# Performance work log

Measured on AMD Instinct MI355X. Metric: run time of the kernel, lower is better.

Reference implementation:

```python
import jax, jax.numpy as jnp
import numpy as np

B, R, T, Q = 4096, 130, 200, 64  # batch, ROIs, BOLD length (= feature_nums), query dim
EPS = 1e-5
GCN_DIMS = [(T, 16), (16, 16), (16, 4), (4, 4), (4, 2), (2, 2)]


def bn1d(x, g, b):
    # torch.nn.BatchNorm1d(R) on (B, R, L): channel dim=1, training-mode batch stats, biased var
    m = x.mean(axis=(0, 2), keepdims=True)
    v = ((x - m) ** 2).mean(axis=(0, 2), keepdims=True)
    return g[None, :, None] * (x - m) * jax.lax.rsqrt(v + EPS) + b[None, :, None]


def setup_inputs() -> dict:
    key = jax.random.key(0)
    ks = jax.random.split(key, 16)

    def kaiming(k, shape, fan_in):  # kaiming_normal_ with relu gain
        return (jax.random.normal(k, shape) * np.sqrt(2.0 / fan_in)).astype(jnp.float32)

    inp = {}
    inp['BOLD_signals'] = jax.random.normal(ks[0], (B, R, T), dtype=jnp.float32)
    inp['threshold'] = jnp.float32(0.005)
    inp['wq'] = kaiming(ks[1], (Q, T), T)
    inp['bq'] = jnp.zeros((Q,), jnp.float32)
    inp['g_t'] = jnp.ones((R,), jnp.float32)
    inp['b_t'] = jnp.zeros((R,), jnp.float32)
    for i, (fi, fo) in enumerate(GCN_DIMS, 1):
        inp[f'w{i}'] = kaiming(ks[1 + i], (fo, fi), fi)
        inp[f'b{i}'] = jnp.zeros((fo,), jnp.float32)
        inp[f'g{i}'] = jnp.ones((R,), jnp.float32)
        inp[f'beta{i}'] = jnp.zeros((R,), jnp.float32)
    inp['w_mlp'] = kaiming(ks[9], (2, R * 2), R * 2)
    inp['b_mlp'] = jnp.zeros((2,), jnp.float32)
    return inp


def reference(BOLD_signals, threshold, wq, bq, g_t, b_t,
              w1, b1, g1, beta1, w2, b2, g2, beta2, w3, b3, g3, beta3,
              w4, b4, g4, beta4, w5, b5, g5, beta5, w6, b6, g6, beta6,
              w_mlp, b_mlp):
    x = jnp.where(jnp.isnan(BOLD_signals), 0.0, BOLD_signals)  # (B,R,T)

    # Transformer-style relation matrix (note: K is a reshape, not a transpose, per source)
    qk = x @ wq.T + bq                      # (B,R,Q)
    Qm = qk.reshape(-1, R, Q)               # (B,R,Q)
    Km = qk.reshape(-1, Q, R)               # (B,Q,R)  -- faithful reshape
    rel = jnp.einsum('brq,bqs->brs', Qm, Km)  # (B,R,R)
    rel = bn1d(rel, g_t, b_t)
    rel = jax.nn.softmax(rel, axis=2)
    rel = jax.nn.relu(rel - threshold)

    def gcn(A, f, w, b, g, beta):
        return jax.nn.relu(bn1d(A @ f @ w.T + b, g, beta))

    h = gcn(rel, x, w1, b1, g1, beta1)           # (B,R,16)
    h = gcn(rel, h, w2, b2, g2, beta2) + h       # res
    h = gcn(rel, h, w3, b3, g3, beta3)           # (B,R,4)
    h = gcn(rel, h, w4, b4, g4, beta4) + h       # res
    h = gcn(rel, h, w5, b5, g5, beta5)           # (B,R,2)
    h = gcn(rel, h, w6, b6, g6, beta6) + h       # res

    out = jax.nn.relu(h.reshape(h.shape[0], -1) @ w_mlp.T + b_mlp)  # (B,2)
    return out
```

## Files before the change

### kernel.cpp

```cpp
#include <hip/hip_runtime.h>
#include <math.h>


typedef _Float16 f16;
typedef _Float16 f16x8 __attribute__((ext_vector_type(8)));
typedef _Float16 f16x4 __attribute__((ext_vector_type(4)));
typedef float f32x4 __attribute__((ext_vector_type(4)));

#define MFMA16(a, b, c) __builtin_amdgcn_mfma_f32_16x16x32_f16((a), (b), (c), 0, 0, 0)

__global__ __launch_bounds__(256) void w_prep(
    const float* __restrict__ wq, const float* __restrict__ w1, f16* __restrict__ wf)
{
  const int f = blockIdx.x;
  const int k = threadIdx.x;
  if (k < 224) {
    float v = 0.f;
    if (k < 200) v = (f < 64) ? wq[f * 200 + k] : w1[(f - 64) * 200 + k];
    wf[f * 224 + k] = (f16)v;
  }
}

__global__ __launch_bounds__(256) void k_in(
    const float* __restrict__ x, const f16* __restrict__ wf,
    const float* __restrict__ bq, f16* __restrict__ qk, f16* __restrict__ xw1)
{
  __shared__ f16 xs[64 * 232];
  const int tid = threadIdx.x;
  const size_t m0 = (size_t)blockIdx.x * 64;
  {
    int r = tid >> 2, j = tid & 3;
    *(float4*)&xs[r * 232 + 200 + j * 8] = make_float4(0, 0, 0, 0);
  }
  const float4* xsrc = (const float4*)(x + m0 * 200);
  for (int i = tid; i < 3200; i += 256) {
    int r = i / 50, c = i - (i / 50) * 50;
    float4 v = xsrc[i];
    v.x = (v.x != v.x) ? 0.f : v.x;
    v.y = (v.y != v.y) ? 0.f : v.y;
    v.z = (v.z != v.z) ? 0.f : v.z;
    v.w = (v.w != v.w) ? 0.f : v.w;
    f16x4 h; h[0] = (f16)v.x; h[1] = (f16)v.y; h[2] = (f16)v.z; h[3] = (f16)v.w;
    *(f16x4*)&xs[r * 232 + c * 4] = h;
  }
  __syncthreads();
  const int lane = tid & 63, wv = tid >> 6;
  const int mrow = lane & 15, quad = lane >> 4;
  f32x4 acc[5];
#pragma unroll
  for (int n = 0; n < 5; n++) acc[n] = (f32x4){0.f, 0.f, 0.f, 0.f};
  const f16* xrow = &xs[(wv * 16 + mrow) * 232 + quad * 8];
  const f16* wrow = wf + mrow * 224 + quad * 8;
#pragma unroll
  for (int k0 = 0; k0 < 224; k0 += 32) {
    f16x8 af = *(const f16x8*)(xrow + k0);
#pragma unroll
    for (int n = 0; n < 5; n++)
      acc[n] = MFMA16(af, *(const f16x8*)(wrow + n * 3584 + k0), acc[n]);
  }
  const size_t rbase = m0 + wv * 16;
#pragma unroll
  for (int n = 0; n < 4; n++) {
    int col = n * 16 + mrow;
    float bqv = bq[col];
#pragma unroll
    for (int i = 0; i < 4; i++)
      qk[(rbase + quad * 4 + i) * 64 + col] = (f16)(acc[n][i] + bqv);
  }
#pragma unroll
  for (int i = 0; i < 4; i++)
    xw1[(rbase + quad * 4 + i) * 16 + mrow] = (f16)acc[4][i];
}

__device__ __forceinline__ void gather_bfrags(const f16* qf, int mrow, int quad,
                                              f16x8 bf[9][2])
{
#pragma unroll
  for (int n = 0; n < 9; n++) {
    const int s = n * 16 + mrow;
    const bool ok = (s < 130);
#pragma unroll
    for (int kh = 0; kh < 2; kh++) {
      f16x8 t;
#pragma unroll
      for (int j = 0; j < 8; j++) {
        int q = kh * 32 + quad * 8 + j;
        t[j] = ok ? qf[q * 130 + s] : (f16)0.f;
      }
      bf[n][kh] = t;
    }
  }
}

__global__ __launch_bounds__(256) void k_relstats(
    const f16* __restrict__ qk, float* __restrict__ sp)
{
  __shared__ f16 qf[8320];
  const int b = blockIdx.x, tid = threadIdx.x;
  const f16* qb = qk + (size_t)b * 8320;
  for (int i = tid; i < 1040; i += 256)
    *(f16x8*)&qf[i * 8] = *(const f16x8*)(qb + i * 8);
  __syncthreads();
  const int lane = tid & 63, wv = tid >> 6, mrow = lane & 15, quad = lane >> 4;
  f16x8 bf[9][2];
  gather_bfrags(qf, mrow, quad, bf);
  for (int m = wv; m < 9; m += 4) {
    const f16* arow = qb + (m * 16 + mrow) * 64 + quad * 8;
    f16x8 af0 = *(const f16x8*)arow;
    f16x8 af1 = *(const f16x8*)(arow + 32);
    float p1[4] = {0, 0, 0, 0}, p2[4] = {0, 0, 0, 0};
#pragma unroll
    for (int n = 0; n < 9; n++) {
      f32x4 acc = (f32x4){0.f, 0.f, 0.f, 0.f};
      acc = MFMA16(af0, bf[n][0], acc);
      acc = MFMA16(af1, bf[n][1], acc);
#pragma unroll
      for (int i = 0; i < 4; i++) { float v = acc[i]; p1[i] += v; p2[i] += v * v; }
    }
#pragma unroll
    for (int i = 0; i < 4; i++)
#pragma unroll
      for (int msk = 1; msk <= 8; msk <<= 1) {
        p1[i] += __shfl_xor(p1[i], msk); p2[i] += __shfl_xor(p2[i], msk);
      }
    if (mrow == 0) {
#pragma unroll
      for (int i = 0; i < 4; i++) {
        int r = m * 16 + quad * 4 + i;
        if (r < 130) {
          sp[(size_t)r * 4096 + b] = p1[i];
          sp[130 * 4096 + (size_t)r * 4096 + b] = p2[i];
        }
      }
    }
  }
}

__global__ __launch_bounds__(256) void k_stats(
    const float* __restrict__ sp, const float* __restrict__ g,
    const float* __restrict__ beta, float invN, float* __restrict__ ac)
{
  const int r = blockIdx.x, tid = threadIdx.x;
  float s1 = 0.f, s2 = 0.f;
  const float* p1 = sp + (size_t)r * 4096;
  const float* p2 = sp + 130 * 4096 + (size_t)r * 4096;
  for (int j = tid; j < 4096; j += 256) { s1 += p1[j]; s2 += p2[j]; }
#pragma unroll
  for (int m = 1; m <= 32; m <<= 1) { s1 += __shfl_xor(s1, m); s2 += __shfl_xor(s2, m); }
  __shared__ float r1[4], r2[4];
  if ((tid & 63) == 0) { r1[tid >> 6] = s1; r2[tid >> 6] = s2; }
  __syncthreads();
  if (tid == 0) {
    float S1 = r1[0] + r1[1] + r1[2] + r1[3];
    float S2 = r2[0] + r2[1] + r2[2] + r2[3];
    float mean = S1 * invN;
    float var = S2 * invN - mean * mean;
    float a = g[r] * rsqrtf(var + 1e-5f);
    ac[r] = a;
    ac[130 + r] = beta[r] - mean * a;
  }
}

__global__ __launch_bounds__(256) void k_Asoft(
    const f16* __restrict__ qk, const float* __restrict__ ac0,
    const float* __restrict__ thrp, f16* __restrict__ A16)
{
  __shared__ f16 qf[8320];
  const int b = blockIdx.x, tid = threadIdx.x;
  const f16* qb = qk + (size_t)b * 8320;
  for (int i = tid; i < 1040; i += 256)
    *(f16x8*)&qf[i * 8] = *(const f16x8*)(qb + i * 8);
  __syncthreads();
  const float thr = *thrp;
  const int lane = tid & 63, wv = tid >> 6, mrow = lane & 15, quad = lane >> 4;
  f16x8 bf[9][2];
  gather_bfrags(qf, mrow, quad, bf);
  f16* Ab = A16 + (size_t)b * 17680;
  for (int m = wv; m < 9; m += 4) {
    float a4[4], c4[4];
#pragma unroll
    for (int i = 0; i < 4; i++) {
      int r = m * 16 + quad * 4 + i;
      a4[i] = (r < 130) ? ac0[r] : 0.f;
      c4[i] = (r < 130) ? ac0[130 + r] : 0.f;
    }
    const f16* arow = qb + (m * 16 + mrow) * 64 + quad * 8;
    f16x8 af0 = *(const f16x8*)arow;
    f16x8 af1 = *(const f16x8*)(arow + 32);
    f32x4 acc[9];
#pragma unroll
    for (int n = 0; n < 9; n++) {
      acc[n] = (f32x4){0.f, 0.f, 0.f, 0.f};
      acc[n] = MFMA16(af0, bf[n][0], acc[n]);
      acc[n] = MFMA16(af1, bf[n][1], acc[n]);
    }
    float mx[4] = {-3e38f, -3e38f, -3e38f, -3e38f}, sm[4] = {0, 0, 0, 0};
#pragma unroll
    for (int n = 0; n < 9; n++) {
      const bool valid = (n * 16 + mrow) < 130;
#pragma unroll
      for (int i = 0; i < 4; i++) {
        float v = a4[i] * acc[n][i] + c4[i];
        float ve = valid ? v : -3e38f;
        float nm = fmaxf(mx[i], ve);
        sm[i] = sm[i] * __expf(mx[i] - nm) + (valid ? __expf(v - nm) : 0.f);
        mx[i] = nm;
      }
    }
#pragma unroll
    for (int i = 0; i < 4; i++) {
#pragma unroll
      for (int msk = 1; msk <= 8; msk <<= 1) {
        float om = __shfl_xor(mx[i], msk), os = __shfl_xor(sm[i], msk);
        float nm = fmaxf(mx[i], om);
        sm[i] = sm[i] * __expf(mx[i] - nm) + os * __expf(om - nm);
        mx[i] = nm;
      }
      sm[i] = 1.f / sm[i];
    }
#pragma unroll
    for (int n = 0; n < 9; n++) {
      const int col = n * 16 + mrow;
#pragma unroll
      for (int i = 0; i < 4; i++) {
        int r = m * 16 + quad * 4 + i;
        if (r < 130) {
          if (col < 130) {
            float v = a4[i] * acc[n][i] + c4[i];
            Ab[r * 136 + col] = (f16)fmaxf(__expf(v - mx[i]) * sm[i] - thr, 0.f);
          } else if (col < 136) {
            Ab[r * 136 + col] = (f16)0.f;
          }
        }
      }
    }
  }
}

template <int FI, int FO, bool RES, bool G1>
__global__ __launch_bounds__(256) void k_gcn(
    const f16* __restrict__ A16, const float* __restrict__ ZP,
    const float* __restrict__ ZQ, const f16* __restrict__ xw1,
    const float* __restrict__ acP, const float* __restrict__ acQ,
    const float* __restrict__ wmat, const float* __restrict__ bb,
    float* __restrict__ Zout, float* __restrict__ sp)
{
  __shared__ f16 gT[16 * 168];
  const int b = blockIdx.x, tid = threadIdx.x;
  for (int i = tid; i < 1344; i += 256) ((float*)gT)[i] = 0.f;
  __syncthreads();
  if constexpr (G1) {
    for (int i = tid; i < 2080; i += 256) {
      int s = i >> 4, f = i & 15;
      gT[f * 168 + s] = xw1[(size_t)b * 2080 + i];
    }
  } else {
    if (tid < 130) {
      const int r = tid;
      float h[FI];
      const float* zp = ZP + ((size_t)b * 130 + r) * FI;
      const float aP = acP[r], cP = acP[130 + r];
#pragma unroll
      for (int i = 0; i < FI; i++) h[i] = fmaxf(aP * zp[i] + cP, 0.f);
      if constexpr (RES) {
        const float* zq = ZQ + ((size_t)b * 130 + r) * FI;
        const float aQ = acQ[r], cQ = acQ[130 + r];
#pragma unroll
        for (int i = 0; i < FI; i++) h[i] += fmaxf(aQ * zq[i] + cQ, 0.f);
      }
#pragma unroll
      for (int k = 0; k < FO; k++) {
        float s = 0.f;
#pragma unroll
        for (int i = 0; i < FI; i++) s += h[i] * wmat[k * FI + i];
        gT[k * 168 + r] = (f16)s;
      }
    }
  }
  __syncthreads();
  const int lane = tid & 63, wv = tid >> 6, mrow = lane & 15, quad = lane >> 4;
  f16x8 bfr[5];
#pragma unroll
  for (int kk = 0; kk < 5; kk++)
    bfr[kk] = *(const f16x8*)&gT[mrow * 168 + kk * 32 + quad * 8];
  const f16* Ab = A16 + (size_t)b * 17680;
  for (int m = wv; m < 9; m += 4) {
    const f16* arow = Ab + (m * 16 + mrow) * 136 + quad * 8;
    f32x4 acc = (f32x4){0.f, 0.f, 0.f, 0.f};
#pragma unroll
    for (int kk = 0; kk < 5; kk++)
      acc = MFMA16(*(const f16x8*)(arow + kk * 32), bfr[kk], acc);
    const int col = mrow;
    const float bk = (col < FO) ? bb[col] : 0.f;
    float p1[4], p2[4];
#pragma unroll
    for (int i = 0; i < 4; i++) {
      int r = m * 16 + quad * 4 + i;
      float v = (col < FO) ? acc[i] + bk : 0.f;
      if (col < FO && r < 130)
        Zout[((size_t)b * 130 + r) * FO + col] = v;
      p1[i] = v; p2[i] = v * v;
    }
#pragma unroll
    for (int i = 0; i < 4; i++)
#pragma unroll
      for (int msk = 1; msk <= 8; msk <<= 1) {
        p1[i] += __shfl_xor(p1[i], msk); p2[i] += __shfl_xor(p2[i], msk);
      }
    if (mrow == 0) {
#pragma unroll
      for (int i = 0; i < 4; i++) {
        int r = m * 16 + quad * 4 + i;
        if (r < 130) {
          sp[(size_t)r * 4096 + b] = p1[i];
          sp[130 * 4096 + (size_t)r * 4096 + b] = p2[i];
        }
      }
    }
  }
}

__global__ __launch_bounds__(256) void k_mlp(
    const float* __restrict__ Z5, const float* __restrict__ Z6,
    const float* __restrict__ ac5, const float* __restrict__ ac6,
    const float* __restrict__ wm, const float* __restrict__ bm, float* __restrict__ out)
{
  const int tid = threadIdx.x, lane = tid & 63, wv = tid >> 6;
  const int b = blockIdx.x * 4 + wv;
  const float* z5 = Z5 + (size_t)b * 260;
  const float* z6 = Z6 + (size_t)b * 260;
  float p0 = 0.f, p1 = 0.f;
#pragma unroll
  for (int j = 0; j < 5; j++) {
    int i = lane + 64 * j;
    if (i < 260) {
      int r = i >> 1;
      float h = fmaxf(ac6[r] * z6[i] + ac6[130 + r], 0.f)
              + fmaxf(ac5[r] * z5[i] + ac5[130 + r], 0.f);
      p0 += h * wm[i];
      p1 += h * wm[260 + i];
    }
  }
#pragma unroll
  for (int m = 1; m <= 32; m <<= 1) { p0 += __shfl_xor(p0, m); p1 += __shfl_xor(p1, m); }
  if (lane == 0) {
    out[(size_t)b * 2] = fmaxf(p0 + bm[0], 0.f);
    out[(size_t)b * 2 + 1] = fmaxf(p1 + bm[1], 0.f);
  }
}

extern "C" void kernel_launch(void* const* d_in, const int* in_sizes, int n_in,
                              void* d_out, int out_size, void* d_ws, size_t ws_size,
                              hipStream_t stream) {
  const float* X   = (const float*)d_in[0];
  const float* THR = (const float*)d_in[1];
  const float* WQ  = (const float*)d_in[2];
  const float* BQ  = (const float*)d_in[3];
  const float* GT  = (const float*)d_in[4];
  const float* BT  = (const float*)d_in[5];
  const float* W1 = (const float*)d_in[6];  const float* Bb1 = (const float*)d_in[7];
  const float* G1g = (const float*)d_in[8]; const float* BE1 = (const float*)d_in[9];
  const float* W2 = (const float*)d_in[10]; const float* Bb2 = (const float*)d_in[11];
  const float* G2 = (const float*)d_in[12]; const float* BE2 = (const float*)d_in[13];
  const float* W3 = (const float*)d_in[14]; const float* Bb3 = (const float*)d_in[15];
  const float* G3 = (const float*)d_in[16]; const float* BE3 = (const float*)d_in[17];
  const float* W4 = (const float*)d_in[18]; const float* Bb4 = (const float*)d_in[19];
  const float* G4 = (const float*)d_in[20]; const float* BE4 = (const float*)d_in[21];
  const float* W5 = (const float*)d_in[22]; const float* Bb5 = (const float*)d_in[23];
  const float* G5 = (const float*)d_in[24]; const float* BE5 = (const float*)d_in[25];
  const float* W6 = (const float*)d_in[26]; const float* Bb6 = (const float*)d_in[27];
  const float* G6 = (const float*)d_in[28]; const float* BE6 = (const float*)d_in[29];
  const float* WM = (const float*)d_in[30]; const float* BM = (const float*)d_in[31];

  float* ws = (float*)d_ws;
  f16*   A16   = (f16*)ws;
  f16*   qk16  = (f16*)(ws + 36208640);
  f16*   xw116 = (f16*)(ws + 53248000);
  f16*   wf16  = (f16*)(ws + 57507840);
  float* Z1 = ws + 57516800;
  float* Z2 = ws + 66036480;
  float* Z3 = ws + 74556160;
  float* Z4 = ws + 76686080;
  float* Z5 = ws + 78816000;
  float* Z6 = ws + 79880960;
  float* sp = ws + 80945920;
  float* ac = ws + 82010880;

  w_prep<<<80, 256, 0, stream>>>(WQ, W1, wf16);
  k_in<<<8320, 256, 0, stream>>>(X, wf16, BQ, qk16, xw116);
  k_relstats<<<4096, 256, 0, stream>>>(qk16, sp);
  k_stats<<<130, 256, 0, stream>>>(sp, GT, BT, 1.f / 532480.f, ac);
  k_Asoft<<<4096, 256, 0, stream>>>(qk16, ac, THR, A16);
  k_gcn<16, 16, false, true><<<4096, 256, 0, stream>>>(A16, nullptr, nullptr, xw116,
      nullptr, nullptr, nullptr, Bb1, Z1, sp);
  k_stats<<<130, 256, 0, stream>>>(sp, G1g, BE1, 1.f / 65536.f, ac + 260);
  k_gcn<16, 16, false, false><<<4096, 256, 0, stream>>>(A16, Z1, nullptr, nullptr,
      ac + 260, nullptr, W2, Bb2, Z2, sp);
  k_stats<<<130, 256, 0, stream>>>(sp, G2, BE2, 1.f / 65536.f, ac + 520);
  k_gcn<16, 4, true, false><<<4096, 256, 0, stream>>>(A16, Z2, Z1, nullptr,
      ac + 520, ac + 260, W3, Bb3, Z3, sp);
  k_stats<<<130, 256, 0, stream>>>(sp, G3, BE3, 1.f / 16384.f, ac + 780);
  k_gcn<4, 4, false, false><<<4096, 256, 0, stream>>>(A16, Z3, nullptr, nullptr,
      ac + 780, nullptr, W4, Bb4, Z4, sp);
  k_stats<<<130, 256, 0, stream>>>(sp, G4, BE4, 1.f / 16384.f, ac + 1040);
  k_gcn<4, 2, true, false><<<4096, 256, 0, stream>>>(A16, Z4, Z3, nullptr,
      ac + 1040, ac + 780, W5, Bb5, Z5, sp);
  k_stats<<<130, 256, 0, stream>>>(sp, G5, BE5, 1.f / 8192.f, ac + 1300);
  k_gcn<2, 2, false, false><<<4096, 256, 0, stream>>>(A16, Z5, nullptr, nullptr,
      ac + 1300, nullptr, W6, Bb6, Z6, sp);
  k_stats<<<130, 256, 0, stream>>>(sp, G6, BE6, 1.f / 8192.f, ac + 1560);
  k_mlp<<<1024, 256, 0, stream>>>(Z5, Z6, ac + 1300, ac + 1560, WM, BM, (float*)d_out);
}
```

Before: 1.136 ms.

## Fuse all stages into one persistent cooperative kernel with grid syncs

Replaces the sequence of separate kernel launches with a single cooperative persistent kernel. Blocks loop over work items and use grid-wide barriers between phases, which removes per-launch overhead and tail gaps between the many small stats and GCN kernels. The input projection now reads X directly from global memory instead of staging it in LDS. The softmax is reworked into a three-pass recompute (max, sum, write) that repeats the small MFMAs instead of keeping all accumulators in registers. In exchange, occupancy is capped at a fixed grid, the 130-block stats phases leave most blocks idle at barriers, and the extra MFMA passes add compute.

```diff
diff --git a/kernel.cpp b/kernel.cpp
--- a/kernel.cpp
+++ b/kernel.cpp
@@ -1,76 +1,29 @@
 #include <hip/hip_runtime.h>
+#include <hip/hip_cooperative_groups.h>
 #include <math.h>
+
+namespace cg = cooperative_groups;
 
 
 typedef _Float16 f16;
 typedef _Float16 f16x8 __attribute__((ext_vector_type(8)));
-typedef _Float16 f16x4 __attribute__((ext_vector_type(4)));
 typedef float f32x4 __attribute__((ext_vector_type(4)));
 
 #define MFMA16(a, b, c) __builtin_amdgcn_mfma_f32_16x16x32_f16((a), (b), (c), 0, 0, 0)
 
-__global__ __launch_bounds__(256) void w_prep(
-    const float* __restrict__ wq, const float* __restrict__ w1, f16* __restrict__ wf)
-{
-  const int f = blockIdx.x;
-  const int k = threadIdx.x;
-  if (k < 224) {
-    float v = 0.f;
-    if (k < 200) v = (f < 64) ? wq[f * 200 + k] : w1[(f - 64) * 200 + k];
-    wf[f * 224 + k] = (f16)v;
-  }
-}
-
-__global__ __launch_bounds__(256) void k_in(
-    const float* __restrict__ x, const f16* __restrict__ wf,
-    const float* __restrict__ bq, f16* __restrict__ qk, f16* __restrict__ xw1)
-{
-  __shared__ f16 xs[64 * 232];
-  const int tid = threadIdx.x;
-  const size_t m0 = (size_t)blockIdx.x * 64;
-  {
-    int r = tid >> 2, j = tid & 3;
-    *(float4*)&xs[r * 232 + 200 + j * 8] = make_float4(0, 0, 0, 0);
-  }
-  const float4* xsrc = (const float4*)(x + m0 * 200);
-  for (int i = tid; i < 3200; i += 256) {
-    int r = i / 50, c = i - (i / 50) * 50;
-    float4 v = xsrc[i];
-    v.x = (v.x != v.x) ? 0.f : v.x;
-    v.y = (v.y != v.y) ? 0.f : v.y;
-    v.z = (v.z != v.z) ? 0.f : v.z;
-    v.w = (v.w != v.w) ? 0.f : v.w;
-    f16x4 h; h[0] = (f16)v.x; h[1] = (f16)v.y; h[2] = (f16)v.z; h[3] = (f16)v.w;
-    *(f16x4*)&xs[r * 232 + c * 4] = h;
-  }
-  __syncthreads();
-  const int lane = tid & 63, wv = tid >> 6;
-  const int mrow = lane & 15, quad = lane >> 4;
-  f32x4 acc[5];
-#pragma unroll
-  for (int n = 0; n < 5; n++) acc[n] = (f32x4){0.f, 0.f, 0.f, 0.f};
-  const f16* xrow = &xs[(wv * 16 + mrow) * 232 + quad * 8];
-  const f16* wrow = wf + mrow * 224 + quad * 8;
-#pragma unroll
-  for (int k0 = 0; k0 < 224; k0 += 32) {
-    f16x8 af = *(const f16x8*)(xrow + k0);
-#pragma unroll
-    for (int n = 0; n < 5; n++)
-      acc[n] = MFMA16(af, *(const f16x8*)(wrow + n * 3584 + k0), acc[n]);
-  }
-  const size_t rbase = m0 + wv * 16;
-#pragma unroll
-  for (int n = 0; n < 4; n++) {
-    int col = n * 16 + mrow;
-    float bqv = bq[col];
-#pragma unroll
-    for (int i = 0; i < 4; i++)
-      qk[(rbase + quad * 4 + i) * 64 + col] = (f16)(acc[n][i] + bqv);
-  }
-#pragma unroll
-  for (int i = 0; i < 4; i++)
-    xw1[(rbase + quad * 4 + i) * 16 + mrow] = (f16)acc[4][i];
-}
+struct Params {
+  const float *X, *THR, *WQ, *BQ, *GT, *BT;
+  const float *W1, *Bb1, *G1, *BE1;
+  const float *W2, *Bb2, *G2, *BE2;
+  const float *W3, *Bb3, *G3, *BE3;
+  const float *W4, *Bb4, *G4, *BE4;
+  const float *W5, *Bb5, *G5, *BE5;
+  const float *W6, *Bb6, *G6, *BE6;
+  const float *WM, *BM;
+  f16 *A16, *qk, *xw1, *wf;
+  float *Z1, *Z2, *Z3, *Z4, *Z5, *Z6, *sp, *ac;
+  float *out;
+};
 
 __device__ __forceinline__ void gather_bfrags(const f16* qf, int mrow, int quad,
                                               f16x8 bf[9][2])
@@ -92,144 +45,289 @@
   }
 }
 
-__global__ __launch_bounds__(256) void k_relstats(
-    const f16* __restrict__ qk, float* __restrict__ sp)
-{
-  __shared__ f16 qf[8320];
-  const int b = blockIdx.x, tid = threadIdx.x;
-  const f16* qb = qk + (size_t)b * 8320;
-  for (int i = tid; i < 1040; i += 256)
-    *(f16x8*)&qf[i * 8] = *(const f16x8*)(qb + i * 8);
-  __syncthreads();
+__device__ void kin_phase(const float* __restrict__ X, const f16* __restrict__ wf,
+                          const float* __restrict__ bq, f16* __restrict__ qk,
+                          f16* __restrict__ xw1, int bid, int nb, int tid)
+{
   const int lane = tid & 63, wv = tid >> 6, mrow = lane & 15, quad = lane >> 4;
-  f16x8 bf[9][2];
-  gather_bfrags(qf, mrow, quad, bf);
-  for (int m = wv; m < 9; m += 4) {
-    const f16* arow = qb + (m * 16 + mrow) * 64 + quad * 8;
-    f16x8 af0 = *(const f16x8*)arow;
-    f16x8 af1 = *(const f16x8*)(arow + 32);
-    float p1[4] = {0, 0, 0, 0}, p2[4] = {0, 0, 0, 0};
-#pragma unroll
-    for (int n = 0; n < 9; n++) {
-      f32x4 acc = (f32x4){0.f, 0.f, 0.f, 0.f};
-      acc = MFMA16(af0, bf[n][0], acc);
-      acc = MFMA16(af1, bf[n][1], acc);
-#pragma unroll
-      for (int i = 0; i < 4; i++) { float v = acc[i]; p1[i] += v; p2[i] += v * v; }
+  const int cbase = quad * 8;
+  for (int t = bid; t < 8320; t += nb) {
+    const size_t m0 = (size_t)t * 64;
+    const float* xr = X + (m0 + wv * 16 + mrow) * 200;
+    f32x4 acc[5];
+#pragma unroll
+    for (int n = 0; n < 5; n++) acc[n] = (f32x4){0.f, 0.f, 0.f, 0.f};
+#pragma unroll
+    for (int k0 = 0; k0 < 224; k0 += 32) {
+      const int c0 = k0 + cbase;
+      f16x8 af;
+#pragma unroll
+      for (int j = 0; j < 8; j++) af[j] = (f16)0.f;
+      if (c0 < 200) {
+        float4 v0 = *(const float4*)(xr + c0);
+        float4 v1 = *(const float4*)(xr + c0 + 4);
+        float vv[8];
+        *(float4*)&vv[0] = v0;
+        *(float4*)&vv[4] = v1;
+#pragma unroll
+        for (int j = 0; j < 8; j++) {
+          float x = vv[j];
+          af[j] = (f16)((x != x) ? 0.f : x);
+        }
+      }
+#pragma unroll
+      for (int n = 0; n < 5; n++)
+        acc[n] = MFMA16(af, *(const f16x8*)(wf + (n * 16 + mrow) * 224 + c0), acc[n]);
+    }
+    const size_t rbase = m0 + wv * 16;
+#pragma unroll
+    for (int n = 0; n < 4; n++) {
+      int col = n * 16 + mrow;
+      float bqv = bq[col];
+#pragma unroll
+      for (int i = 0; i < 4; i++)
+        qk[(rbase + quad * 4 + i) * 64 + col] = (f16)(acc[n][i] + bqv);
     }
 #pragma unroll
     for (int i = 0; i < 4; i++)
-#pragma unroll
-      for (int msk = 1; msk <= 8; msk <<= 1) {
-        p1[i] += __shfl_xor(p1[i], msk); p2[i] += __shfl_xor(p2[i], msk);
-      }
-    if (mrow == 0) {
+      xw1[(rbase + quad * 4 + i) * 16 + mrow] = (f16)acc[4][i];
+  }
+}
+
+__device__ void relstats_phase(const f16* __restrict__ qk, float* __restrict__ sp,
+                               f16* qf, int bid, int nb, int tid)
+{
+  const int lane = tid & 63, wv = tid >> 6, mrow = lane & 15, quad = lane >> 4;
+  for (int b = bid; b < 4096; b += nb) {
+    __syncthreads();
+    const f16* qb = qk + (size_t)b * 8320;
+    for (int i = tid; i < 1040; i += 256)
+      *(f16x8*)&qf[i * 8] = *(const f16x8*)(qb + i * 8);
+    __syncthreads();
+    f16x8 bf[9][2];
+    gather_bfrags(qf, mrow, quad, bf);
+    for (int m = wv; m < 9; m += 4) {
+      const f16* arow = qb + (m * 16 + mrow) * 64 + quad * 8;
+      f16x8 af0 = *(const f16x8*)arow;
+      f16x8 af1 = *(const f16x8*)(arow + 32);
+      float p1[4] = {0, 0, 0, 0}, p2[4] = {0, 0, 0, 0};
+#pragma unroll
+      for (int n = 0; n < 9; n++) {
+        f32x4 acc = (f32x4){0.f, 0.f, 0.f, 0.f};
+        acc = MFMA16(af0, bf[n][0], acc);
+        acc = MFMA16(af1, bf[n][1], acc);
+#pragma unroll
+        for (int i = 0; i < 4; i++) { float v = acc[i]; p1[i] += v; p2[i] += v * v; }
+      }
+#pragma unroll
+      for (int i = 0; i < 4; i++)
+#pragma unroll
+        for (int msk = 1; msk <= 8; msk <<= 1) {
+          p1[i] += __shfl_xor(p1[i], msk); p2[i] += __shfl_xor(p2[i], msk);
+        }
+      if (mrow == 0) {
+#pragma unroll
+        for (int i = 0; i < 4; i++) {
+          int r = m * 16 + quad * 4 + i;
+          if (r < 130) {
+            sp[(size_t)r * 4096 + b] = p1[i];
+            sp[130 * 4096 + (size_t)r * 4096 + b] = p2[i];
+          }
+        }
+      }
+    }
+  }
+}
+
+__device__ void stats_phase(const float* __restrict__ sp, const float* __restrict__ g,
+                            const float* __restrict__ be, float invN,
+                            float* __restrict__ acOut, float* rr, int bid, int tid)
+{
+  if (bid < 130) {
+    const int r = bid;
+    float s1 = 0.f, s2 = 0.f;
+    const float* p1 = sp + (size_t)r * 4096;
+    const float* p2 = sp + 130 * 4096 + (size_t)r * 4096;
+    for (int j = tid; j < 4096; j += 256) { s1 += p1[j]; s2 += p2[j]; }
+#pragma unroll
+    for (int m = 1; m <= 32; m <<= 1) { s1 += __shfl_xor(s1, m); s2 += __shfl_xor(s2, m); }
+    if ((tid & 63) == 0) { rr[tid >> 6] = s1; rr[4 + (tid >> 6)] = s2; }
+    __syncthreads();
+    if (tid == 0) {
+      float S1 = rr[0] + rr[1] + rr[2] + rr[3];
+      float S2 = rr[4] + rr[5] + rr[6] + rr[7];
+      float mean = S1 * invN;
+      float var = S2 * invN - mean * mean;
+      float a = g[r] * rsqrtf(var + 1e-5f);
+      acOut[r] = a;
+      acOut[130 + r] = be[r] - mean * a;
+    }
+  }
+}
+
+__device__ void asoft_phase(const f16* __restrict__ qk, const float* __restrict__ ac0,
+                            float thr, f16* __restrict__ A16, f16* qf,
+                            int bid, int nb, int tid)
+{
+  const int lane = tid & 63, wv = tid >> 6, mrow = lane & 15, quad = lane >> 4;
+  for (int b = bid; b < 4096; b += nb) {
+    __syncthreads();
+    const f16* qb = qk + (size_t)b * 8320;
+    for (int i = tid; i < 1040; i += 256)
+      *(f16x8*)&qf[i * 8] = *(const f16x8*)(qb + i * 8);
+    __syncthreads();
+    f16x8 bf[9][2];
+    gather_bfrags(qf, mrow, quad, bf);
+    f16* Ab = A16 + (size_t)b * 17680;
+    for (int m = wv; m < 9; m += 4) {
+      float a4[4], c4[4];
 #pragma unroll
       for (int i = 0; i < 4; i++) {
         int r = m * 16 + quad * 4 + i;
-        if (r < 130) {
-          sp[(size_t)r * 4096 + b] = p1[i];
-          sp[130 * 4096 + (size_t)r * 4096 + b] = p2[i];
-        }
-      }
-    }
-  }
-}
-
-__global__ __launch_bounds__(256) void k_stats(
-    const float* __restrict__ sp, const float* __restrict__ g,
-    const float* __restrict__ beta, float invN, float* __restrict__ ac)
-{
-  const int r = blockIdx.x, tid = threadIdx.x;
-  float s1 = 0.f, s2 = 0.f;
-  const float* p1 = sp + (size_t)r * 4096;
-  const float* p2 = sp + 130 * 4096 + (size_t)r * 4096;
-  for (int j = tid; j < 4096; j += 256) { s1 += p1[j]; s2 += p2[j]; }
-#pragma unroll
-  for (int m = 1; m <= 32; m <<= 1) { s1 += __shfl_xor(s1, m); s2 += __shfl_xor(s2, m); }
-  __shared__ float r1[4], r2[4];
-  if ((tid & 63) == 0) { r1[tid >> 6] = s1; r2[tid >> 6] = s2; }
-  __syncthreads();
-  if (tid == 0) {
-    float S1 = r1[0] + r1[1] + r1[2] + r1[3];
-    float S2 = r2[0] + r2[1] + r2[2] + r2[3];
-    float mean = S1 * invN;
-    float var = S2 * invN - mean * mean;
-    float a = g[r] * rsqrtf(var + 1e-5f);
-    ac[r] = a;
-    ac[130 + r] = beta[r] - mean * a;
-  }
-}
-
-__global__ __launch_bounds__(256) void k_Asoft(
-    const f16* __restrict__ qk, const float* __restrict__ ac0,
-    const float* __restrict__ thrp, f16* __restrict__ A16)
-{
-  __shared__ f16 qf[8320];
-  const int b = blockIdx.x, tid = threadIdx.x;
-  const f16* qb = qk + (size_t)b * 8320;
-  for (int i = tid; i < 1040; i += 256)
-    *(f16x8*)&qf[i * 8] = *(const f16x8*)(qb + i * 8);
-  __syncthreads();
-  const float thr = *thrp;
+        a4[i] = (r < 130) ? ac0[r] : 0.f;
+        c4[i] = (r < 130) ? ac0[130 + r] : 0.f;
+      }
+      const f16* arow = qb + (m * 16 + mrow) * 64 + quad * 8;
+      f16x8 af0 = *(const f16x8*)arow;
+      f16x8 af1 = *(const f16x8*)(arow + 32);
+      float mx[4] = {-3e38f, -3e38f, -3e38f, -3e38f};
+#pragma unroll
+      for (int n = 0; n < 9; n++) {
+        f32x4 acc = (f32x4){0.f, 0.f, 0.f, 0.f};
+        acc = MFMA16(af0, bf[n][0], acc);
+        acc = MFMA16(af1, bf[n][1], acc);
+        const bool valid = (n * 16 + mrow) < 130;
+#pragma unroll
+        for (int i = 0; i < 4; i++) {
+          float v = a4[i] * acc[i] + c4[i];
+          if (valid) mx[i] = fmaxf(mx[i], v);
+        }
+      }
+#pragma unroll
+      for (int i = 0; i < 4; i++)
+#pragma unroll
+        for (int msk = 1; msk <= 8; msk <<= 1)
+          mx[i] = fmaxf(mx[i], __shfl_xor(mx[i], msk));
+      float sm[4] = {0.f, 0.f, 0.f, 0.f};
+#pragma unroll
+      for (int n = 0; n < 9; n++) {
+        f32x4 acc = (f32x4){0.f, 0.f, 0.f, 0.f};
+        acc = MFMA16(af0, bf[n][0], acc);
+        acc = MFMA16(af1, bf[n][1], acc);
+        const bool valid = (n * 16 + mrow) < 130;
+#pragma unroll
+        for (int i = 0; i < 4; i++) {
+          float v = a4[i] * acc[i] + c4[i];
+          if (valid) sm[i] += __expf(v - mx[i]);
+        }
+      }
+#pragma unroll
+      for (int i = 0; i < 4; i++) {
+#pragma unroll
+        for (int msk = 1; msk <= 8; msk <<= 1)
+          sm[i] += __shfl_xor(sm[i], msk);
+        sm[i] = 1.f / sm[i];
+      }
+#pragma unroll
+      for (int n = 0; n < 9; n++) {
+        f32x4 acc = (f32x4){0.f, 0.f, 0.f, 0.f};
+        acc = MFMA16(af0, bf[n][0], acc);
+        acc = MFMA16(af1, bf[n][1], acc);
+        const int col = n * 16 + mrow;
+#pragma unroll
+        for (int i = 0; i < 4; i++) {
+          int r = m * 16 + quad * 4 + i;
+          if (r < 130) {
+            if (col < 130) {
+              float v = a4[i] * acc[i] + c4[i];
+              Ab[r * 136 + col] = (f16)fmaxf(__expf(v - mx[i]) * sm[i] - thr, 0.f);
+            } else if (col < 136) {
+              Ab[r * 136 + col] = (f16)0.f;
+            }
+          }
+        }
+      }
+    }
+  }
+}
+
+template <int FI, int FO, bool RES, bool G1f>
+__device__ void gcn_phase(const f16* __restrict__ A16, const float* __restrict__ ZP,
+                          const float* __restrict__ ZQ, const f16* __restrict__ xw1,
+                          const float* __restrict__ acP, const float* __restrict__ acQ,
+                          const float* __restrict__ wmat, const float* __restrict__ bb,
+                          float* __restrict__ Zout, float* __restrict__ sp,
+                          f16* gT, int bid, int nb, int tid)
+{
   const int lane = tid & 63, wv = tid >> 6, mrow = lane & 15, quad = lane >> 4;
-  f16x8 bf[9][2];
-  gather_bfrags(qf, mrow, quad, bf);
-  f16* Ab = A16 + (size_t)b * 17680;
-  for (int m = wv; m < 9; m += 4) {
-    float a4[4], c4[4];
-#pragma unroll
-    for (int i = 0; i < 4; i++) {
-      int r = m * 16 + quad * 4 + i;
-      a4[i] = (r < 130) ? ac0[r] : 0.f;
-      c4[i] = (r < 130) ? ac0[130 + r] : 0.f;
-    }
-    const f16* arow = qb + (m * 16 + mrow) * 64 + quad * 8;
-    f16x8 af0 = *(const f16x8*)arow;
-    f16x8 af1 = *(const f16x8*)(arow + 32);
-    f32x4 acc[9];
-#pragma unroll
-    for (int n = 0; n < 9; n++) {
-      acc[n] = (f32x4){0.f, 0.f, 0.f, 0.f};
-      acc[n] = MFMA16(af0, bf[n][0], acc[n]);
-      acc[n] = MFMA16(af1, bf[n][1], acc[n]);
-    }
-    float mx[4] = {-3e38f, -3e38f, -3e38f, -3e38f}, sm[4] = {0, 0, 0, 0};
-#pragma unroll
-    for (int n = 0; n < 9; n++) {
-      const bool valid = (n * 16 + mrow) < 130;
-#pragma unroll
-      for (int i = 0; i < 4; i++) {
-        float v = a4[i] * acc[n][i] + c4[i];
-        float ve = valid ? v : -3e38f;
-        float nm = fmaxf(mx[i], ve);
-        sm[i] = sm[i] * __expf(mx[i] - nm) + (valid ? __expf(v - nm) : 0.f);
-        mx[i] = nm;
-      }
-    }
-#pragma unroll
-    for (int i = 0; i < 4; i++) {
-#pragma unroll
-      for (int msk = 1; msk <= 8; msk <<= 1) {
-        float om = __shfl_xor(mx[i], msk), os = __shfl_xor(sm[i], msk);
-        float nm = fmaxf(mx[i], om);
-        sm[i] = sm[i] * __expf(mx[i] - nm) + os * __expf(om - nm);
-        mx[i] = nm;
-      }
-      sm[i] = 1.f / sm[i];
-    }
-#pragma unroll
-    for (int n = 0; n < 9; n++) {
-      const int col = n * 16 + mrow;
+  for (int b = bid; b < 4096; b += nb) {
+    __syncthreads();
+    for (int i = tid; i < 1344; i += 256) ((float*)gT)[i] = 0.f;
+    __syncthreads();
+    if constexpr (G1f) {
+      for (int i = tid; i < 2080; i += 256) {
+        int s = i >> 4, f = i & 15;
+        gT[f * 168 + s] = xw1[(size_t)b * 2080 + i];
+      }
+    } else {
+      if (tid < 130) {
+        const int r = tid;
+        float h[FI];
+        const float* zp = ZP + ((size_t)b * 130 + r) * FI;
+        const float aP = acP[r], cP = acP[130 + r];
+#pragma unroll
+        for (int i = 0; i < FI; i++) h[i] = fmaxf(aP * zp[i] + cP, 0.f);
+        if constexpr (RES) {
+          const float* zq = ZQ + ((size_t)b * 130 + r) * FI;
+          const float aQ = acQ[r], cQ = acQ[130 + r];
+#pragma unroll
+          for (int i = 0; i < FI; i++) h[i] += fmaxf(aQ * zq[i] + cQ, 0.f);
+        }
+#pragma unroll
+        for (int k = 0; k < FO; k++) {
+          float s = 0.f;
+#pragma unroll
+          for (int i = 0; i < FI; i++) s += h[i] * wmat[k * FI + i];
+          gT[k * 168 + r] = (f16)s;
+        }
+      }
+    }
+    __syncthreads();
+    f16x8 bfr[5];
+#pragma unroll
+    for (int kk = 0; kk < 5; kk++)
+      bfr[kk] = *(const f16x8*)&gT[mrow * 168 + kk * 32 + quad * 8];
+    const f16* Ab = A16 + (size_t)b * 17680;
+    for (int m = wv; m < 9; m += 4) {
+      const f16* arow = Ab + (m * 16 + mrow) * 136 + quad * 8;
+      f32x4 acc = (f32x4){0.f, 0.f, 0.f, 0.f};
+#pragma unroll
+      for (int kk = 0; kk < 5; kk++)
+        acc = MFMA16(*(const f16x8*)(arow + kk * 32), bfr[kk], acc);
+      const int col = mrow;
+      const float bk = (col < FO) ? bb[col] : 0.f;
+      float p1[4], p2[4];
 #pragma unroll
       for (int i = 0; i < 4; i++) {
         int r = m * 16 + quad * 4 + i;
-        if (r < 130) {
-          if (col < 130) {
-            float v = a4[i] * acc[n][i] + c4[i];
-            Ab[r * 136 + col] = (f16)fmaxf(__expf(v - mx[i]) * sm[i] - thr, 0.f);
-          } else if (col < 136) {
-            Ab[r * 136 + col] = (f16)0.f;
+        float v = (col < FO) ? acc[i] + bk : 0.f;
+        if (col < FO && r < 130)
+          Zout[((size_t)b * 130 + r) * FO + col] = v;
+        p1[i] = v; p2[i] = v * v;
+      }
+#pragma unroll
+      for (int i = 0; i < 4; i++)
+#pragma unroll
+        for (int msk = 1; msk <= 8; msk <<= 1) {
+          p1[i] += __shfl_xor(p1[i], msk); p2[i] += __shfl_xor(p2[i], msk);
+        }
+      if (mrow == 0) {
+#pragma unroll
+        for (int i = 0; i < 4; i++) {
+          int r = m * 16 + quad * 4 + i;
+          if (r < 130) {
+            sp[(size_t)r * 4096 + b] = p1[i];
+            sp[130 * 4096 + (size_t)r * 4096 + b] = p2[i];
           }
         }
       }
@@ -237,177 +335,138 @@
   }
 }
 
-template <int FI, int FO, bool RES, bool G1>
-__global__ __launch_bounds__(256) void k_gcn(
-    const f16* __restrict__ A16, const float* __restrict__ ZP,
-    const float* __restrict__ ZQ, const f16* __restrict__ xw1,
-    const float* __restrict__ acP, const float* __restrict__ acQ,
-    const float* __restrict__ wmat, const float* __restrict__ bb,
-    float* __restrict__ Zout, float* __restrict__ sp)
-{
-  __shared__ f16 gT[16 * 168];
-  const int b = blockIdx.x, tid = threadIdx.x;
-  for (int i = tid; i < 1344; i += 256) ((float*)gT)[i] = 0.f;
-  __syncthreads();
-  if constexpr (G1) {
-    for (int i = tid; i < 2080; i += 256) {
-      int s = i >> 4, f = i & 15;
-      gT[f * 168 + s] = xw1[(size_t)b * 2080 + i];
-    }
-  } else {
-    if (tid < 130) {
-      const int r = tid;
-      float h[FI];
-      const float* zp = ZP + ((size_t)b * 130 + r) * FI;
-      const float aP = acP[r], cP = acP[130 + r];
-#pragma unroll
-      for (int i = 0; i < FI; i++) h[i] = fmaxf(aP * zp[i] + cP, 0.f);
-      if constexpr (RES) {
-        const float* zq = ZQ + ((size_t)b * 130 + r) * FI;
-        const float aQ = acQ[r], cQ = acQ[130 + r];
-#pragma unroll
-        for (int i = 0; i < FI; i++) h[i] += fmaxf(aQ * zq[i] + cQ, 0.f);
-      }
-#pragma unroll
-      for (int k = 0; k < FO; k++) {
-        float s = 0.f;
-#pragma unroll
-        for (int i = 0; i < FI; i++) s += h[i] * wmat[k * FI + i];
-        gT[k * 168 + r] = (f16)s;
-      }
-    }
-  }
-  __syncthreads();
-  const int lane = tid & 63, wv = tid >> 6, mrow = lane & 15, quad = lane >> 4;
-  f16x8 bfr[5];
-#pragma unroll
-  for (int kk = 0; kk < 5; kk++)
-    bfr[kk] = *(const f16x8*)&gT[mrow * 168 + kk * 32 + quad * 8];
-  const f16* Ab = A16 + (size_t)b * 17680;
-  for (int m = wv; m < 9; m += 4) {
-    const f16* arow = Ab + (m * 16 + mrow) * 136 + quad * 8;
-    f32x4 acc = (f32x4){0.f, 0.f, 0.f, 0.f};
-#pragma unroll
-    for (int kk = 0; kk < 5; kk++)
-      acc = MFMA16(*(const f16x8*)(arow + kk * 32), bfr[kk], acc);
-    const int col = mrow;
-    const float bk = (col < FO) ? bb[col] : 0.f;
-    float p1[4], p2[4];
-#pragma unroll
-    for (int i = 0; i < 4; i++) {
-      int r = m * 16 + quad * 4 + i;
-      float v = (col < FO) ? acc[i] + bk : 0.f;
-      if (col < FO && r < 130)
-        Zout[((size_t)b * 130 + r) * FO + col] = v;
-      p1[i] = v; p2[i] = v * v;
-    }
-#pragma unroll
-    for (int i = 0; i < 4; i++)
-#pragma unroll
-      for (int msk = 1; msk <= 8; msk <<= 1) {
-        p1[i] += __shfl_xor(p1[i], msk); p2[i] += __shfl_xor(p2[i], msk);
-      }
-    if (mrow == 0) {
-#pragma unroll
-      for (int i = 0; i < 4; i++) {
-        int r = m * 16 + quad * 4 + i;
-        if (r < 130) {
-          sp[(size_t)r * 4096 + b] = p1[i];
-          sp[130 * 4096 + (size_t)r * 4096 + b] = p2[i];
-        }
-      }
-    }
-  }
-}
-
-__global__ __launch_bounds__(256) void k_mlp(
-    const float* __restrict__ Z5, const float* __restrict__ Z6,
-    const float* __restrict__ ac5, const float* __restrict__ ac6,
-    const float* __restrict__ wm, const float* __restrict__ bm, float* __restrict__ out)
-{
-  const int tid = threadIdx.x, lane = tid & 63, wv = tid >> 6;
-  const int b = blockIdx.x * 4 + wv;
-  const float* z5 = Z5 + (size_t)b * 260;
-  const float* z6 = Z6 + (size_t)b * 260;
-  float p0 = 0.f, p1 = 0.f;
-#pragma unroll
-  for (int j = 0; j < 5; j++) {
-    int i = lane + 64 * j;
-    if (i < 260) {
-      int r = i >> 1;
-      float h = fmaxf(ac6[r] * z6[i] + ac6[130 + r], 0.f)
-              + fmaxf(ac5[r] * z5[i] + ac5[130 + r], 0.f);
-      p0 += h * wm[i];
-      p1 += h * wm[260 + i];
-    }
-  }
-#pragma unroll
-  for (int m = 1; m <= 32; m <<= 1) { p0 += __shfl_xor(p0, m); p1 += __shfl_xor(p1, m); }
-  if (lane == 0) {
-    out[(size_t)b * 2] = fmaxf(p0 + bm[0], 0.f);
-    out[(size_t)b * 2 + 1] = fmaxf(p1 + bm[1], 0.f);
-  }
+__device__ void mlp_phase(const float* __restrict__ Z5, const float* __restrict__ Z6,
+                          const float* __restrict__ ac5, const float* __restrict__ ac6,
+                          const float* __restrict__ wm, const float* __restrict__ bm,
+                          float* __restrict__ out, int bid, int nb, int tid)
+{
+  const int lane = tid & 63, wv = tid >> 6;
+  for (int b = bid * 4 + wv; b < 4096; b += nb * 4) {
+    const float* z5 = Z5 + (size_t)b * 260;
+    const float* z6 = Z6 + (size_t)b * 260;
+    float p0 = 0.f, p1 = 0.f;
+#pragma unroll
+    for (int j = 0; j < 5; j++) {
+      int i = lane + 64 * j;
+      if (i < 260) {
+        int r = i >> 1;
+        float h = fmaxf(ac6[r] * z6[i] + ac6[130 + r], 0.f)
+                + fmaxf(ac5[r] * z5[i] + ac5[130 + r], 0.f);
+        p0 += h * wm[i];
+        p1 += h * wm[260 + i];
+      }
+    }
+#pragma unroll
+    for (int m = 1; m <= 32; m <<= 1) { p0 += __shfl_xor(p0, m); p1 += __shfl_xor(p1, m); }
+    if (lane == 0) {
+      out[(size_t)b * 2] = fmaxf(p0 + bm[0], 0.f);
+      out[(size_t)b * 2 + 1] = fmaxf(p1 + bm[1], 0.f);
+    }
+  }
+}
+
+__global__ __launch_bounds__(256, 4) void mega(Params P, int nb)
+{
+  cg::grid_group grid = cg::this_grid();
+  __shared__ __align__(16) char smemraw[16640];
+  f16* qf = (f16*)smemraw;
+  f16* gT = (f16*)smemraw;
+  float* rr = (float*)smemraw;
+  const int bid = blockIdx.x, tid = threadIdx.x;
+
+  for (int idx = bid * 256 + tid; idx < 80 * 224; idx += nb * 256) {
+    int f = idx / 224, k = idx - f * 224;
+    float v = 0.f;
+    if (k < 200) v = (f < 64) ? P.WQ[f * 200 + k] : P.W1[(f - 64) * 200 + k];
+    P.wf[idx] = (f16)v;
+  }
+  grid.sync();
+  kin_phase(P.X, P.wf, P.BQ, P.qk, P.xw1, bid, nb, tid);
+  grid.sync();
+  relstats_phase(P.qk, P.sp, qf, bid, nb, tid);
+  grid.sync();
+  stats_phase(P.sp, P.GT, P.BT, 1.f / 532480.f, P.ac, rr, bid, tid);
+  grid.sync();
+  const float thr = *P.THR;
+  asoft_phase(P.qk, P.ac, thr, P.A16, qf, bid, nb, tid);
+  grid.sync();
+  gcn_phase<16, 16, false, true>(P.A16, nullptr, nullptr, P.xw1, nullptr, nullptr,
+                                 nullptr, P.Bb1, P.Z1, P.sp, gT, bid, nb, tid);
+  grid.sync();
+  stats_phase(P.sp, P.G1, P.BE1, 1.f / 65536.f, P.ac + 260, rr, bid, tid);
+  grid.sync();
+  gcn_phase<16, 16, false, false>(P.A16, P.Z1, nullptr, nullptr, P.ac + 260, nullptr,
+                                  P.W2, P.Bb2, P.Z2, P.sp, gT, bid, nb, tid);
+  grid.sync();
+  stats_phase(P.sp, P.G2, P.BE2, 1.f / 65536.f, P.ac + 520, rr, bid, tid);
+  grid.sync();
+  gcn_phase<16, 4, true, false>(P.A16, P.Z2, P.Z1, nullptr, P.ac + 520, P.ac + 260,
+                                P.W3, P.Bb3, P.Z3, P.sp, gT, bid, nb, tid);
+  grid.sync();
+  stats_phase(P.sp, P.G3, P.BE3, 1.f / 16384.f, P.ac + 780, rr, bid, tid);
+  grid.sync();
+  gcn_phase<4, 4, false, false>(P.A16, P.Z3, nullptr, nullptr, P.ac + 780, nullptr,
+                                P.W4, P.Bb4, P.Z4, P.sp, gT, bid, nb, tid);
+  grid.sync();
+  stats_phase(P.sp, P.G4, P.BE4, 1.f / 16384.f, P.ac + 1040, rr, bid, tid);
+  grid.sync();
+  gcn_phase<4, 2, true, false>(P.A16, P.Z4, P.Z3, nullptr, P.ac + 1040, P.ac + 780,
+                               P.W5, P.Bb5, P.Z5, P.sp, gT, bid, nb, tid);
+  grid.sync();
+  stats_phase(P.sp, P.G5, P.BE5, 1.f / 8192.f, P.ac + 1300, rr, bid, tid);
+  grid.sync();
+  gcn_phase<2, 2, false, false>(P.A16, P.Z5, nullptr, nullptr, P.ac + 1300, nullptr,
+                                P.W6, P.Bb6, P.Z6, P.sp, gT, bid, nb, tid);
+  grid.sync();
+  stats_phase(P.sp, P.G6, P.BE6, 1.f / 8192.f, P.ac + 1560, rr, bid, tid);
+  grid.sync();
+  mlp_phase(P.Z5, P.Z6, P.ac + 1300, P.ac + 1560, P.WM, P.BM, P.out, bid, nb, tid);
 }
 
 extern "C" void kernel_launch(void* const* d_in, const int* in_sizes, int n_in,
                               void* d_out, int out_size, void* d_ws, size_t ws_size,
                               hipStream_t stream) {
-  const float* X   = (const float*)d_in[0];
-  const float* THR = (const float*)d_in[1];
-  const float* WQ  = (const float*)d_in[2];
-  const float* BQ  = (const float*)d_in[3];
-  const float* GT  = (const float*)d_in[4];
-  const float* BT  = (const float*)d_in[5];
-  const float* W1 = (const float*)d_in[6];  const float* Bb1 = (const float*)d_in[7];
-  const float* G1g = (const float*)d_in[8]; const float* BE1 = (const float*)d_in[9];
-  const float* W2 = (const float*)d_in[10]; const float* Bb2 = (const float*)d_in[11];
-  const float* G2 = (const float*)d_in[12]; const float* BE2 = (const float*)d_in[13];
-  const float* W3 = (const float*)d_in[14]; const float* Bb3 = (const float*)d_in[15];
-  const float* G3 = (const float*)d_in[16]; const float* BE3 = (const float*)d_in[17];
-  const float* W4 = (const float*)d_in[18]; const float* Bb4 = (const float*)d_in[19];
-  const float* G4 = (const float*)d_in[20]; const float* BE4 = (const float*)d_in[21];
-  const float* W5 = (const float*)d_in[22]; const float* Bb5 = (const float*)d_in[23];
-  const float* G5 = (const float*)d_in[24]; const float* BE5 = (const float*)d_in[25];
-  const float* W6 = (const float*)d_in[26]; const float* Bb6 = (const float*)d_in[27];
-  const float* G6 = (const float*)d_in[28]; const float* BE6 = (const float*)d_in[29];
-  const float* WM = (const float*)d_in[30]; const float* BM = (const float*)d_in[31];
+  Params P;
+  P.X   = (const float*)d_in[0];
+  P.THR = (const float*)d_in[1];
+  P.WQ  = (const float*)d_in[2];
+  P.BQ  = (const float*)d_in[3];
+  P.GT  = (const float*)d_in[4];
+  P.BT  = (const float*)d_in[5];
+  P.W1 = (const float*)d_in[6];  P.Bb1 = (const float*)d_in[7];
+  P.G1 = (const float*)d_in[8];  P.BE1 = (const float*)d_in[9];
+  P.W2 = (const float*)d_in[10]; P.Bb2 = (const float*)d_in[11];
+  P.G2 = (const float*)d_in[12]; P.BE2 = (const float*)d_in[13];
+  P.W3 = (const float*)d_in[14]; P.Bb3 = (const float*)d_in[15];
+  P.G3 = (const float*)d_in[16]; P.BE3 = (const float*)d_in[17];
+  P.W4 = (const float*)d_in[18]; P.Bb4 = (const float*)d_in[19];
+  P.G4 = (const float*)d_in[20]; P.BE4 = (const float*)d_in[21];
+  P.W5 = (const float*)d_in[22]; P.Bb5 = (const float*)d_in[23];
+  P.G5 = (const float*)d_in[24]; P.BE5 = (const float*)d_in[25];
+  P.W6 = (const float*)d_in[26]; P.Bb6 = (const float*)d_in[27];
+  P.G6 = (const float*)d_in[28]; P.BE6 = (const float*)d_in[29];
+  P.WM = (const float*)d_in[30]; P.BM = (const float*)d_in[31];
 
   float* ws = (float*)d_ws;
-  f16*   A16   = (f16*)ws;
-  f16*   qk16  = (f16*)(ws + 36208640);
-  f16*   xw116 = (f16*)(ws + 53248000);
-  f16*   wf16  = (f16*)(ws + 57507840);
-  float* Z1 = ws + 57516800;
-  float* Z2 = ws + 66036480;
-  float* Z3 = ws + 74556160;
-  float* Z4 = ws + 76686080;
-  float* Z5 = ws + 78816000;
-  float* Z6 = ws + 79880960;
-  float* sp = ws + 80945920;
-  float* ac = ws + 82010880;
-
-  w_prep<<<80, 256, 0, stream>>>(WQ, W1, wf16);
-  k_in<<<8320, 256, 0, stream>>>(X, wf16, BQ, qk16, xw116);
-  k_relstats<<<4096, 256, 0, stream>>>(qk16, sp);
-  k_stats<<<130, 256, 0, stream>>>(sp, GT, BT, 1.f / 532480.f, ac);
-  k_Asoft<<<4096, 256, 0, stream>>>(qk16, ac, THR, A16);
-  k_gcn<16, 16, false, true><<<4096, 256, 0, stream>>>(A16, nullptr, nullptr, xw116,
-      nullptr, nullptr, nullptr, Bb1, Z1, sp);
-  k_stats<<<130, 256, 0, stream>>>(sp, G1g, BE1, 1.f / 65536.f, ac + 260);
-  k_gcn<16, 16, false, false><<<4096, 256, 0, stream>>>(A16, Z1, nullptr, nullptr,
-      ac + 260, nullptr, W2, Bb2, Z2, sp);
-  k_stats<<<130, 256, 0, stream>>>(sp, G2, BE2, 1.f / 65536.f, ac + 520);
-  k_gcn<16, 4, true, false><<<4096, 256, 0, stream>>>(A16, Z2, Z1, nullptr,
-      ac + 520, ac + 260, W3, Bb3, Z3, sp);
-  k_stats<<<130, 256, 0, stream>>>(sp, G3, BE3, 1.f / 16384.f, ac + 780);
-  k_gcn<4, 4, false, false><<<4096, 256, 0, stream>>>(A16, Z3, nullptr, nullptr,
-      ac + 780, nullptr, W4, Bb4, Z4, sp);
-  k_stats<<<130, 256, 0, stream>>>(sp, G4, BE4, 1.f / 16384.f, ac + 1040);
-  k_gcn<4, 2, true, false><<<4096, 256, 0, stream>>>(A16, Z4, Z3, nullptr,
-      ac + 1040, ac + 780, W5, Bb5, Z5, sp);
-  k_stats<<<130, 256, 0, stream>>>(sp, G5, BE5, 1.f / 8192.f, ac + 1300);
-  k_gcn<2, 2, false, false><<<4096, 256, 0, stream>>>(A16, Z5, nullptr, nullptr,
-      ac + 1300, nullptr, W6, Bb6, Z6, sp);
-  k_stats<<<130, 256, 0, stream>>>(sp, G6, BE6, 1.f / 8192.f, ac + 1560);
-  k_mlp<<<1024, 256, 0, stream>>>(Z5, Z6, ac + 1300, ac + 1560, WM, BM, (float*)d_out);
-}
+  P.A16  = (f16*)ws;
+  P.qk   = (f16*)(ws + 36208640);
+  P.xw1  = (f16*)(ws + 53248000);
+  P.wf   = (f16*)(ws + 57507840);
+  P.Z1 = ws + 57516800;
+  P.Z2 = ws + 66036480;
+  P.Z3 = ws + 74556160;
+  P.Z4 = ws + 76686080;
+  P.Z5 = ws + 78816000;
+  P.Z6 = ws + 79880960;
+  P.sp = ws + 80945920;
+  P.ac = ws + 82010880;
+  P.out = (float*)d_out;
+
+  int occ = 0;
+  hipError_t e = hipOccupancyMaxActiveBlocksPerMultiprocessor(&occ, mega, 256, 0);
+  if (e != hipSuccess || occ < 1) occ = 1;
+  int nb = occ * 256;
+  if (nb > 4096) nb = 4096;
+  void* args[] = { (void*)&P, (void*)&nb };
+  hipLaunchCooperativeKernel((void*)mega, dim3(nb), dim3(256), args, 0, stream);
+}
```

Result: slower. 2.517 ms (+121.6%).
